# Performance work log

Measured on AMD Instinct MI355X. Metric: run time of the kernel, lower is better.

Reference implementation:

```python
import jax, jax.numpy as jnp
import numpy as np

B, S, D, H, I, E, K, L, C = 4, 1024, 512, 8, 2048, 8, 2, 4, 4
D2 = D // 2
EPS = 1e-5  # torch LayerNorm default


def _ln(x, w, b):
    m = jnp.mean(x, -1, keepdims=True)
    v = jnp.mean((x - m) ** 2, -1, keepdims=True)
    return (x - m) * jax.lax.rsqrt(v + EPS) * w + b


def setup_inputs() -> dict:
    key = jax.random.key(0)
    ks = iter(jax.random.split(key, 40))
    n = lambda shp, s=0.02: jax.random.normal(next(ks), shp, dtype=jnp.float32) * s
    return {
        'embeddings': jax.random.normal(next(ks), (B, S, D), jnp.float32),
        'attention_mask': jnp.ones((B, S), jnp.float32),
        'in_w': n((L, 3 * D, D)), 'in_b': jnp.zeros((L, 3 * D)),
        'out_w': n((L, D, D)), 'out_b': jnp.zeros((L, D)),
        'ln1_w': jnp.ones((L, D)), 'ln1_b': jnp.zeros((L, D)),
        'ln2_w': jnp.ones((L, D)), 'ln2_b': jnp.zeros((L, D)),
        'gate_w': n((L, E, D)),
        'e_w1': n((L, E, D, I)), 'e_b1': jnp.zeros((L, E, I)),
        'e_w2': n((L, E, I, D)), 'e_b2': jnp.zeros((L, E, D)),
        'mln_w': jnp.ones((L, D)), 'mln_b': jnp.zeros((L, D)),
        'fln_w': jnp.ones((D,)), 'fln_b': jnp.zeros((D,)),
        'pool_w': n((D, D)), 'pool_b': jnp.zeros((D,)),
        'cls_w': n((C, D)), 'cls_b': jnp.zeros((C,)),
        'cf_w1': n((D2, D)), 'cf_b1': jnp.zeros((D2,)),
        'cf_w2': n((1, D2)), 'cf_b2': jnp.zeros((1,)),
    }


def _forward(embeddings, attention_mask, in_w, in_b, out_w, out_b, ln1_w, ln1_b,
             ln2_w, ln2_b, gate_w, e_w1, e_b1, e_w2, e_b2, mln_w, mln_b,
             fln_w, fln_b, pool_w, pool_b, cls_w, cls_b, cf_w1, cf_b1, cf_w2, cf_b2):
    x = embeddings
    dh = D // H
    total_aux = jnp.float32(0.0)
    for l in range(L):
        # --- self-attention (eval mode, dropout off) ---
        h = _ln(x, ln1_w[l], ln1_b[l])
        qkv = h @ in_w[l].T + in_b[l]                       # (B,S,3D)
        q, k, v = jnp.split(qkv, 3, axis=-1)
        q = q.reshape(B, S, H, dh).transpose(0, 2, 1, 3)
        k = k.reshape(B, S, H, dh).transpose(0, 2, 1, 3)
        v = v.reshape(B, S, H, dh).transpose(0, 2, 1, 3)
        scores = jnp.einsum('bhqd,bhkd->bhqk', q, k) / (dh ** 0.5)
        attn = jax.nn.softmax(scores, axis=-1)
        ctx = jnp.einsum('bhqk,bhkd->bhqd', attn, v).transpose(0, 2, 1, 3).reshape(B, S, D)
        x = x + (ctx @ out_w[l].T + out_b[l])
        # --- MoE FFN (residual is the post-norm2 tensor, per source) ---
        h = _ln(x, ln2_w[l], ln2_b[l])
        flat = h.reshape(-1, D)                             # (T,D)
        probs = jax.nn.softmax(flat @ gate_w[l].T, axis=-1) # (T,E)
        vals, idx = jax.lax.top_k(probs, K)                 # (T,K)
        vals = vals / vals.sum(-1, keepdims=True)
        onehot = jax.nn.one_hot(idx, E, dtype=flat.dtype)   # (T,K,E)
        comb = jnp.einsum('tk,tke->te', vals, onehot)       # (T,E) per-expert weight, 0 if not selected
        mid = jax.nn.gelu(jnp.einsum('td,edf->tef', flat, e_w1[l]) + e_b1[l], approximate=False)
        eout = jnp.einsum('tef,efd->ted', mid, e_w2[l]) + e_b2[l]
        moe_out = jnp.einsum('ted,te->td', eout, comb).reshape(B, S, D)
        moe_out = moe_out * attention_mask[..., None]
        x = _ln(h + moe_out, mln_w[l], mln_b[l])
        usage = onehot.sum((0, 1)) / flat.shape[0]
        total_aux = total_aux + jnp.mean((usage - 1.0 / E) ** 2)
    # --- head ---
    x = _ln(x, fln_w, fln_b)
    me = attention_mask[..., None]
    pooled = (x * me).sum(1) / jnp.maximum(me.sum(1), 1e-9)
    pooled = jnp.tanh(pooled @ pool_w.T + pool_b)
    logits = pooled @ cls_w.T + cls_b
    conf = jax.nn.sigmoid(jax.nn.relu(pooled @ cf_w1.T + cf_b1) @ cf_w2.T + cf_b2)
    return logits, total_aux / L, conf


def reference(embeddings, attention_mask, in_w, in_b, out_w, out_b, ln1_w, ln1_b,
              ln2_w, ln2_b, gate_w, e_w1, e_b1, e_w2, e_b2, mln_w, mln_b,
              fln_w, fln_b, pool_w, pool_b, cls_w, cls_b, cf_w1, cf_b1, cf_w2, cf_b2):
    return _forward(embeddings, attention_mask, in_w, in_b, out_w, out_b, ln1_w, ln1_b,
                    ln2_w, ln2_b, gate_w, e_w1, e_b1, e_w2, e_b2, mln_w, mln_b,
                    fln_w, fln_b, pool_w, pool_b, cls_w, cls_b, cf_w1, cf_b1, cf_w2, cf_b2)
```

## Files before the change

kernel.cpp:

```cpp
#include <hip/hip_runtime.h>
#include <math.h>

#define B_ 4
#define S_ 1024
#define D_ 512
#define H_ 8
#define DH_ 64
#define I_ 2048
#define E_ 8
#define L_ 4
#define T_ 4096

using bf16x8 = __attribute__((ext_vector_type(8))) __bf16;
using f32x4  = __attribute__((ext_vector_type(4))) float;

typedef __attribute__((address_space(1))) const void gvoid;
typedef __attribute__((address_space(3))) void lvoid;
__device__ __forceinline__ void gl_lds16(const void* g, void* l){
  __builtin_amdgcn_global_load_lds((gvoid*)g, (lvoid*)l, 16, 0, 0);
}

__device__ __forceinline__ float wred_sum(float v){
#pragma unroll
  for(int m=32;m>0;m>>=1) v += __shfl_xor(v, m, 64);
  return v;
}
__device__ __forceinline__ unsigned short f2bf(float f){
  unsigned x = __float_as_uint(f);
  unsigned r = (x + 0x7FFFu + ((x>>16)&1u)) >> 16;
  return (unsigned short)r;
}
__device__ __forceinline__ float bf2f(unsigned short u){
  return __uint_as_float(((unsigned)u)<<16);
}
__device__ __forceinline__ unsigned pk2(float a, float b){
  return (unsigned)f2bf(a) | ((unsigned)f2bf(b)<<16);
}

template<int BM, int BN, bool MOE, bool GATHER, bool OUT_BF16, int ACT, bool ADD_IN>
__global__ __launch_bounds__(512)
void gemm_k(const unsigned short* __restrict__ A, const unsigned short* __restrict__ Bv,
            void* Cp, const float* __restrict__ bias, const float* addin,
            int M, int N, int K, int lda, int ldb, int ldc,
            int hdiv, long sAb, long sAh, long sBb, long sBh, long sCb, long sCh,
            float scale,
            const int* __restrict__ moff, const int* __restrict__ mcnt,
            const int* __restrict__ rowtok, const int* __restrict__ btab,
            long sBe, int biasStride, int nby)
{
  constexpr int BK = 64;
  constexpr int WM = BM/2, WN = BN/4, FM = WM/16, FNN = WN/16;
  constexpr int RPC = 64;
  constexpr int SHPC = 4096;
  constexpr int NA = BM/RPC, NB = BN/RPC;
  __shared__ unsigned short As[2*BM*BK];
  __shared__ unsigned short Bs[2*BN*BK];

  const int tid = threadIdx.x, wid = tid>>6, lane = tid&63;
  const int wy = wid>>2, wx = wid&3, ln16 = lane&15;

  const int nwg = gridDim.x, cpx = nwg >> 3;
  const int lin = blockIdx.x;
  const int wg  = (lin & 7)*cpx + (lin >> 3);
  const int bxi = wg / nby, byi = wg % nby;

  int m0 = bxi*BM;
  const int n0 = byi*BN;

  float* Cf = nullptr; unsigned short* Ch = nullptr;
  const float* biasp = bias;
  const unsigned short* Bp = Bv;
  int seg = 0, cnt = M;

  if constexpr (MOE){
    int tv = btab[bxi];
    if (tv < 0) return;
    int e = tv>>8;
    m0 = (tv&255)*BM;
    seg = moff[e]; cnt = mcnt[e];
    Bp = Bv + (long)e*sBe;
    if constexpr (OUT_BF16) Ch = (unsigned short*)Cp; else Cf = (float*)Cp;
    if (biasp) biasp += (long)e*biasStride;
  } else {
    int z = blockIdx.z, zb = z/hdiv, zh = z%hdiv;
    A  += (long)zb*sAb + (long)zh*sAh;
    Bp += (long)zb*sBb + (long)zh*sBh;
    long coff = (long)zb*sCb + (long)zh*sCh;
    if constexpr (OUT_BF16) Ch = (unsigned short*)Cp + coff; else Cf = ((float*)Cp) + coff;
    if constexpr (ADD_IN) addin += coff;
  }

  const int srow = tid >> 3;
  const int scol = ((tid & 7) ^ (srow & 7)) * 8;
  long ga[NA], gb[NB];
#pragma unroll
  for (int j=0; j<NA; j++){
    int r = m0 + j*RPC + srow;
    if constexpr (MOE){
      r = min(r, cnt-1);
      long gr = GATHER ? (long)rowtok[seg+r] : (long)(seg+r);
      ga[j] = gr*lda + scol;
    } else {
      ga[j] = (long)min(r, M-1)*lda + scol;
    }
  }
#pragma unroll
  for (int j=0; j<NB; j++){
    int bn = min(n0 + j*RPC + srow, N-1);
    gb[j] = (long)bn*ldb + scol;
  }

  f32x4 acc[FM][FNN];
#pragma unroll
  for(int i=0;i<FM;i++)
#pragma unroll
    for(int j=0;j<FNN;j++){ f32x4 z = {0.f,0.f,0.f,0.f}; acc[i][j] = z; }

  const int nt = K/BK;
  const int rsw = ln16 & 7;
  const int u0 = ((lane>>4)     ^ rsw) * 8;
  const int u1 = ((4+(lane>>4)) ^ rsw) * 8;

#pragma unroll
  for (int j=0; j<NA; j++) gl_lds16(A + ga[j], As + j*SHPC + wid*512);
#pragma unroll
  for (int j=0; j<NB; j++) gl_lds16(Bp + gb[j], Bs + j*SHPC + wid*512);

  for (int t = 0; t < nt; ++t){
    const int cb = t & 1;
    const unsigned short* Ab = As + cb*BM*BK;
    const unsigned short* Bb = Bs + cb*BN*BK;
    unsigned short* An = As + (cb^1)*BM*BK;
    unsigned short* Bn = Bs + (cb^1)*BN*BK;
    const bool pf = (t+1 < nt);
    const long k0n = (long)(t+1)*BK;

    asm volatile("s_waitcnt vmcnt(0)" ::: "memory");
    __builtin_amdgcn_s_barrier();
    __builtin_amdgcn_sched_barrier(0);

    if (pf){
#pragma unroll
      for (int j=0; j<NA; j++) gl_lds16(A + ga[j] + k0n, An + j*SHPC + wid*512);
    }
    {
      bf16x8 fa[FM], fb[FNN];
#pragma unroll
      for(int i=0;i<FM;i++) fa[i] = *(const bf16x8*)&Ab[(wy*WM + i*16 + ln16)*BK + u0];
#pragma unroll
      for(int j=0;j<FNN;j++) fb[j] = *(const bf16x8*)&Bb[(wx*WN + j*16 + ln16)*BK + u0];
      __builtin_amdgcn_s_setprio(1);
#pragma unroll
      for(int i=0;i<FM;i++)
#pragma unroll
        for(int j=0;j<FNN;j++)
          acc[i][j] = __builtin_amdgcn_mfma_f32_16x16x32_bf16(fa[i], fb[j], acc[i][j], 0, 0, 0);
      __builtin_amdgcn_s_setprio(0);
    }
    if (pf){
#pragma unroll
      for (int j=0; j<NB; j++) gl_lds16(Bp + gb[j] + k0n, Bn + j*SHPC + wid*512);
    }
    {
      bf16x8 fa[FM], fb[FNN];
#pragma unroll
      for(int i=0;i<FM;i++) fa[i] = *(const bf16x8*)&Ab[(wy*WM + i*16 + ln16)*BK + u1];
#pragma unroll
      for(int j=0;j<FNN;j++) fb[j] = *(const bf16x8*)&Bb[(wx*WN + j*16 + ln16)*BK + u1];
      __builtin_amdgcn_s_setprio(1);
#pragma unroll
      for(int i=0;i<FM;i++)
#pragma unroll
        for(int j=0;j<FNN;j++)
          acc[i][j] = __builtin_amdgcn_mfma_f32_16x16x32_bf16(fa[i], fb[j], acc[i][j], 0, 0, 0);
      __builtin_amdgcn_s_setprio(0);
    }
  }

#pragma unroll
  for(int i=0;i<FM;i++){
    int mbase = m0 + wy*WM + i*16 + (lane>>4)*4;
#pragma unroll
    for(int j=0;j<FNN;j++){
      int n = n0 + wx*WN + j*16 + ln16;
      float bv = biasp ? biasp[n] : 0.f;
      f32x4 v = acc[i][j];
#pragma unroll
      for(int r=0;r<4;r++){
        int m = mbase + r;
        if (m < cnt){
          float x = v[r]*scale + bv;
          if constexpr (ACT == 1) x = 0.5f*x*(1.f + erff(x*0.70710678118654752f));
          long ci = (long)(MOE ? seg + m : m)*ldc + n;
          if constexpr (ADD_IN) x += addin[ci];
          if constexpr (OUT_BF16) Ch[ci] = f2bf(x);
          else Cf[ci] = x;
        }
      }
    }
  }
}

__global__ __launch_bounds__(256)
void flash_k(const unsigned short* __restrict__ qkvb, const unsigned short* __restrict__ Vt,
             unsigned short* __restrict__ ctx)
{
  __shared__ unsigned short Pl[4][16*72];
  const int qt = blockIdx.x, z = blockIdx.y, b = z>>3, h = z&7;
  const int wid = threadIdx.x>>6, lane = threadIdx.x&63;
  const int ln16 = lane&15, g = lane>>4;
  const int q0 = qt*64 + wid*16;
  unsigned short* Pw = &Pl[wid][0];

  const unsigned short* Qp = qkvb + (long)(b*1024 + q0 + ln16)*1536 + h*64 + g*8;
  bf16x8 qf0 = *(const bf16x8*)Qp;
  bf16x8 qf1 = *(const bf16x8*)(Qp + 32);
  const unsigned short* Kbase = qkvb + (long)b*1024*1536 + 512 + h*64 + g*8;
  const unsigned short* Vbase = Vt + (long)z*65536 + g*8;

  float m_s[4], l_s[4];
  f32x4 oacc[4];
#pragma unroll
  for(int r=0;r<4;r++){ m_s[r] = -1e30f; l_s[r] = 0.f; }
#pragma unroll
  for(int j=0;j<4;j++){ f32x4 zz = {0.f,0.f,0.f,0.f}; oacc[j] = zz; }

  for (int t = 0; t < 16; ++t){
    bf16x8 kf[4][2], vf[4][2];
#pragma unroll
    for(int j=0;j<4;j++){
      const unsigned short* kp = Kbase + (long)(t*64 + j*16 + ln16)*1536;
      kf[j][0] = *(const bf16x8*)kp;
      kf[j][1] = *(const bf16x8*)(kp + 32);
      const unsigned short* vp = Vbase + (long)(j*16 + ln16)*1024 + t*64;
      vf[j][0] = *(const bf16x8*)vp;
      vf[j][1] = *(const bf16x8*)(vp + 32);
    }
    f32x4 sacc[4];
#pragma unroll
    for(int j=0;j<4;j++){ f32x4 zz = {0.f,0.f,0.f,0.f}; sacc[j] = zz; }
#pragma unroll
    for(int j=0;j<4;j++){
      sacc[j] = __builtin_amdgcn_mfma_f32_16x16x32_bf16(qf0, kf[j][0], sacc[j], 0,0,0);
      sacc[j] = __builtin_amdgcn_mfma_f32_16x16x32_bf16(qf1, kf[j][1], sacc[j], 0,0,0);
    }
#pragma unroll
    for(int j=0;j<4;j++)
#pragma unroll
      for(int r=0;r<4;r++) sacc[j][r] *= 0.125f;
    float alpha[4];
#pragma unroll
    for(int r=0;r<4;r++){
      float mx = fmaxf(fmaxf(sacc[0][r], sacc[1][r]), fmaxf(sacc[2][r], sacc[3][r]));
#pragma unroll
      for(int m=1;m<16;m<<=1) mx = fmaxf(mx, __shfl_xor(mx, m, 64));
      float mn = fmaxf(m_s[r], mx);
      alpha[r] = __expf(m_s[r] - mn);
      m_s[r] = mn;
    }
#pragma unroll
    for(int j=0;j<4;j++)
#pragma unroll
      for(int r=0;r<4;r++) sacc[j][r] = __expf(sacc[j][r] - m_s[r]);
#pragma unroll
    for(int r=0;r<4;r++){
      float rs = sacc[0][r]+sacc[1][r]+sacc[2][r]+sacc[3][r];
#pragma unroll
      for(int m=1;m<16;m<<=1) rs += __shfl_xor(rs, m, 64);
      l_s[r] = l_s[r]*alpha[r] + rs;
    }
#pragma unroll
    for(int j=0;j<4;j++)
#pragma unroll
      for(int r=0;r<4;r++) oacc[j][r] *= alpha[r];
#pragma unroll
    for(int j=0;j<4;j++)
#pragma unroll
      for(int r=0;r<4;r++)
        Pw[(g*4+r)*72 + j*16 + ln16] = f2bf(sacc[j][r]);
    bf16x8 pf0 = *(const bf16x8*)&Pw[ln16*72 + g*8];
    bf16x8 pf1 = *(const bf16x8*)&Pw[ln16*72 + 32 + g*8];
#pragma unroll
    for(int j=0;j<4;j++){
      oacc[j] = __builtin_amdgcn_mfma_f32_16x16x32_bf16(pf0, vf[j][0], oacc[j], 0,0,0);
      oacc[j] = __builtin_amdgcn_mfma_f32_16x16x32_bf16(pf1, vf[j][1], oacc[j], 0,0,0);
    }
  }
#pragma unroll
  for(int r=0;r<4;r++){
    float inv = 1.f/l_s[r];
    long row = (long)(b*1024 + q0 + g*4 + r)*512 + h*64;
#pragma unroll
    for(int j=0;j<4;j++)
      ctx[row + j*16 + ln16] = f2bf(oacc[j][r]*inv);
  }
}

template<bool OUT_BF16>
__global__ __launch_bounds__(256)
void ln_w_k(const float* __restrict__ in, const float* __restrict__ w,
            const float* __restrict__ bb, void* __restrict__ outp)
{
  int row = blockIdx.x*4 + (threadIdx.x>>6), lane = threadIdx.x&63;
  const float4* p = (const float4*)(in + (long)row*512 + lane*8);
  float4 a = p[0], c = p[1];
  float s = a.x+a.y+a.z+a.w + c.x+c.y+c.z+c.w;
  float q = a.x*a.x+a.y*a.y+a.z*a.z+a.w*a.w + c.x*c.x+c.y*c.y+c.z*c.z+c.w*c.w;
  s = wred_sum(s); q = wred_sum(q);
  float mean = s*(1.f/512.f);
  float var  = q*(1.f/512.f) - mean*mean;
  float inv  = rsqrtf(var + 1e-5f);
  const float4* wp = (const float4*)(w + lane*8);
  const float4* bp = (const float4*)(bb + lane*8);
  float4 w0 = wp[0], w1 = wp[1], b0 = bp[0], b1 = bp[1];
  float o0 = (a.x-mean)*inv*w0.x + b0.x, o1 = (a.y-mean)*inv*w0.y + b0.y;
  float o2 = (a.z-mean)*inv*w0.z + b0.z, o3 = (a.w-mean)*inv*w0.w + b0.w;
  float o4 = (c.x-mean)*inv*w1.x + b1.x, o5 = (c.y-mean)*inv*w1.y + b1.y;
  float o6 = (c.z-mean)*inv*w1.z + b1.z, o7 = (c.w-mean)*inv*w1.w + b1.w;
  if constexpr (OUT_BF16){
    *(uint4*)((unsigned short*)outp + (long)row*512 + lane*8) =
      make_uint4(pk2(o0,o1), pk2(o2,o3), pk2(o4,o5), pk2(o6,o7));
  } else {
    float4* op = (float4*)((float*)outp + (long)row*512 + lane*8);
    op[0] = make_float4(o0,o1,o2,o3);
    op[1] = make_float4(o4,o5,o6,o7);
  }
}

__global__ __launch_bounds__(256)
void ln2route_k(const float* __restrict__ in, const float* __restrict__ w,
                const float* __restrict__ bb, unsigned short* __restrict__ h2,
                const float* __restrict__ gw,
                int* __restrict__ tok_e, float* __restrict__ tok_w)
{
  int tok = blockIdx.x*4 + (threadIdx.x>>6), lane = threadIdx.x&63;
  const float4* p = (const float4*)(in + (long)tok*512 + lane*8);
  float4 a = p[0], c = p[1];
  float s = a.x+a.y+a.z+a.w + c.x+c.y+c.z+c.w;
  float q = a.x*a.x+a.y*a.y+a.z*a.z+a.w*a.w + c.x*c.x+c.y*c.y+c.z*c.z+c.w*c.w;
  s = wred_sum(s); q = wred_sum(q);
  float mean = s*(1.f/512.f);
  float var  = q*(1.f/512.f) - mean*mean;
  float inv  = rsqrtf(var + 1e-5f);
  const float4* wp = (const float4*)(w + lane*8);
  const float4* bp = (const float4*)(bb + lane*8);
  float4 w0 = wp[0], w1 = wp[1], b0 = bp[0], b1 = bp[1];
  float o[8];
  o[0] = (a.x-mean)*inv*w0.x + b0.x; o[1] = (a.y-mean)*inv*w0.y + b0.y;
  o[2] = (a.z-mean)*inv*w0.z + b0.z; o[3] = (a.w-mean)*inv*w0.w + b0.w;
  o[4] = (c.x-mean)*inv*w1.x + b1.x; o[5] = (c.y-mean)*inv*w1.y + b1.y;
  o[6] = (c.z-mean)*inv*w1.z + b1.z; o[7] = (c.w-mean)*inv*w1.w + b1.w;
  *(uint4*)(h2 + (long)tok*512 + lane*8) =
    make_uint4(pk2(o[0],o[1]), pk2(o[2],o[3]), pk2(o[4],o[5]), pk2(o[6],o[7]));
  float lg[8];
#pragma unroll
  for(int e=0;e<8;e++){
    const float4* gr = (const float4*)(gw + e*512 + lane*8);
    float4 g0 = gr[0], g1 = gr[1];
    float d = o[0]*g0.x + o[1]*g0.y + o[2]*g0.z + o[3]*g0.w
            + o[4]*g1.x + o[5]*g1.y + o[6]*g1.z + o[7]*g1.w;
    lg[e] = wred_sum(d);
  }
  if (lane == 0){
    float mx = lg[0];
#pragma unroll
    for(int e=1;e<8;e++) mx = fmaxf(mx, lg[e]);
    float pr[8];
#pragma unroll
    for(int e=0;e<8;e++) pr[e] = expf(lg[e]-mx);
    int e0 = 0; float p0 = pr[0];
#pragma unroll
    for(int e=1;e<8;e++) if (pr[e] > p0){ p0 = pr[e]; e0 = e; }
    int e1 = -1; float p1 = -1.f;
#pragma unroll
    for(int e=0;e<8;e++) if (e != e0 && pr[e] > p1){ p1 = pr[e]; e1 = e; }
    float invp = 1.f/(p0+p1);
    tok_e[2*tok] = e0; tok_e[2*tok+1] = e1;
    tok_w[2*tok] = p0*invp; tok_w[2*tok+1] = p1*invp;
  }
}

__global__ __launch_bounds__(1024)
void plan_scatter_k(const int* __restrict__ tok_e, const float* __restrict__ tok_w,
                    int* __restrict__ offs, int* __restrict__ cnts, float* __restrict__ aux,
                    int* __restrict__ btab, int* __restrict__ btab64,
                    int* __restrict__ rowtok, float* __restrict__ roww, int* __restrict__ rowof)
{
  __shared__ int hist[8];
  __shared__ int offsS[8];
  __shared__ int base[8];
  const int t = threadIdx.x;
  if (t < 8) hist[t] = 0;
  __syncthreads();
  int e[8]; float w[8];
#pragma unroll
  for (int i=0;i<8;i++){
    e[i] = tok_e[t + i*1024];
    w[i] = tok_w[t + i*1024];
    atomicAdd(&hist[e[i]], 1);
  }
  __syncthreads();
  if (t == 0){
    int o = 0, idx = 0, idx2 = 0; float a = 0.f;
    for (int ee=0; ee<8; ee++){
      offsS[ee] = o;
      int c = hist[ee];
      o += c;
      float u = (float)c*(1.f/4096.f) - 0.125f;
      a += u*u;
      int nb = (c + 127) >> 7;
      for (int j=0;j<nb;j++) btab[idx++] = (ee<<8)|j;
      int nb2 = (c + 63) >> 6;
      for (int j=0;j<nb2;j++) btab64[idx2++] = (ee<<8)|j;
    }
    while (idx < 80) btab[idx++] = -1;
    while (idx2 < 144) btab64[idx2++] = -1;
    *aux += a*(1.f/8.f);
  }
  __syncthreads();
  if (t < 8){
    cnts[t] = hist[t];
    offs[t] = offsS[t];
    base[t] = offsS[t];
  }
  __syncthreads();
#pragma unroll
  for (int i=0;i<8;i++){
    int pos = atomicAdd(&base[e[i]], 1);
    int gi = t + i*1024;
    rowtok[pos] = gi>>1;
    roww[pos] = w[i];
    rowof[gi] = pos;
  }
}

__global__ __launch_bounds__(256)
void ln_moe_k(const float* __restrict__ eout, const int* __restrict__ rowof,
              const float* __restrict__ roww, const float* __restrict__ mask,
              const unsigned short* __restrict__ h2,
              const float* __restrict__ w, const float* __restrict__ bb,
              float* __restrict__ outp)
{
  int tok = blockIdx.x*4 + (threadIdx.x>>6), lane = threadIdx.x&63;
  int r0 = rowof[2*tok], r1 = rowof[2*tok+1];
  float w0w = roww[r0], w1w = roww[r1], mk = mask[tok];
  const float4* ap = (const float4*)(eout + (long)r0*512 + lane*8);
  const float4* bp2 = (const float4*)(eout + (long)r1*512 + lane*8);
  float4 a0 = ap[0], a1 = ap[1], c0 = bp2[0], c1 = bp2[1];
  uint4 hu = *(const uint4*)(h2 + (long)tok*512 + lane*8);
  const unsigned short* hh = (const unsigned short*)&hu;
  float v[8];
  v[0] = bf2f(hh[0]) + (a0.x*w0w + c0.x*w1w)*mk;
  v[1] = bf2f(hh[1]) + (a0.y*w0w + c0.y*w1w)*mk;
  v[2] = bf2f(hh[2]) + (a0.z*w0w + c0.z*w1w)*mk;
  v[3] = bf2f(hh[3]) + (a0.w*w0w + c0.w*w1w)*mk;
  v[4] = bf2f(hh[4]) + (a1.x*w0w + c1.x*w1w)*mk;
  v[5] = bf2f(hh[5]) + (a1.y*w0w + c1.y*w1w)*mk;
  v[6] = bf2f(hh[6]) + (a1.z*w0w + c1.z*w1w)*mk;
  v[7] = bf2f(hh[7]) + (a1.w*w0w + c1.w*w1w)*mk;
  float s = 0.f, q = 0.f;
#pragma unroll
  for(int i=0;i<8;i++){ s += v[i]; q += v[i]*v[i]; }
  s = wred_sum(s); q = wred_sum(q);
  float mean = s*(1.f/512.f);
  float var  = q*(1.f/512.f) - mean*mean;
  float inv  = rsqrtf(var + 1e-5f);
  const float4* wp = (const float4*)(w + lane*8);
  const float4* bpp = (const float4*)(bb + lane*8);
  float4 w0 = wp[0], w1 = wp[1], b0 = bpp[0], b1 = bpp[1];
  float wv[8] = {w0.x,w0.y,w0.z,w0.w,w1.x,w1.y,w1.z,w1.w};
  float bv[8] = {b0.x,b0.y,b0.z,b0.w,b1.x,b1.y,b1.z,b1.w};
  float4* op = (float4*)(outp + (long)tok*512 + lane*8);
  op[0] = make_float4((v[0]-mean)*inv*wv[0]+bv[0], (v[1]-mean)*inv*wv[1]+bv[1],
                      (v[2]-mean)*inv*wv[2]+bv[2], (v[3]-mean)*inv*wv[3]+bv[3]);
  op[1] = make_float4((v[4]-mean)*inv*wv[4]+bv[4], (v[5]-mean)*inv*wv[5]+bv[5],
                      (v[6]-mean)*inv*wv[6]+bv[6], (v[7]-mean)*inv*wv[7]+bv[7]);
}

__global__ __launch_bounds__(256)
void vt_k(const unsigned short* __restrict__ qkvb, unsigned short* __restrict__ Vt)
{
  __shared__ unsigned short tile[64][80];
  int z = blockIdx.y, b = z>>3, h = z&7;
  int t = threadIdx.x;
  int kk = t>>2, dd = (t&3)*16;
  int dd2 = t>>2, kk2 = (t&3)*16;
  for (int c = 0; c < 4; ++c){
    int k0 = (blockIdx.x*4 + c)*64;
    const unsigned short* p = qkvb + ((long)(b*1024 + k0 + kk))*1536 + 1024 + h*64 + dd;
    uint4 u0 = *(const uint4*)p, u1 = *(const uint4*)(p+8);
    __syncthreads();
    *(uint4*)&tile[kk][dd] = u0;
    *(uint4*)&tile[kk][dd+8] = u1;
    __syncthreads();
    uint4 o0, o1;
    unsigned short* s0 = (unsigned short*)&o0;
    unsigned short* s1 = (unsigned short*)&o1;
#pragma unroll
    for(int j=0;j<8;j++){ s0[j] = tile[kk2+j][dd2]; s1[j] = tile[kk2+8+j][dd2]; }
    unsigned short* o = Vt + (long)z*65536 + (long)dd2*1024 + k0 + kk2;
    *(uint4*)o = o0; *(uint4*)(o+8) = o1;
  }
}

__global__ __launch_bounds__(256)
void transpose_cast_k(const float* __restrict__ in, unsigned short* __restrict__ outp,
                      int R, int C, int ZL)
{
  __shared__ float tile[64][65];
  int t = threadIdx.x;
  int rr = t>>2, cc = (t&3)*16;
  int cc2 = t>>2, rr2 = (t&3)*16;
  int c0 = blockIdx.x*64, r0 = blockIdx.y*64;
  for (int zi = 0; zi < ZL; ++zi){
    long zoff = (long)(blockIdx.z*ZL + zi) * R * C;
    const float* pin = in + zoff + (long)(r0+rr)*C + c0 + cc;
    float4 v0=*(const float4*)pin, v1=*(const float4*)(pin+4), v2=*(const float4*)(pin+8), v3=*(const float4*)(pin+12);
    __syncthreads();
    tile[rr][cc+0]=v0.x; tile[rr][cc+1]=v0.y; tile[rr][cc+2]=v0.z; tile[rr][cc+3]=v0.w;
    tile[rr][cc+4]=v1.x; tile[rr][cc+5]=v1.y; tile[rr][cc+6]=v1.z; tile[rr][cc+7]=v1.w;
    tile[rr][cc+8]=v2.x; tile[rr][cc+9]=v2.y; tile[rr][cc+10]=v2.z; tile[rr][cc+11]=v2.w;
    tile[rr][cc+12]=v3.x; tile[rr][cc+13]=v3.y; tile[rr][cc+14]=v3.z; tile[rr][cc+15]=v3.w;
    __syncthreads();
    unsigned tmp[8];
#pragma unroll
    for(int jj=0;jj<8;jj++)
      tmp[jj] = pk2(tile[rr2+2*jj][cc2], tile[rr2+2*jj+1][cc2]);
    uint4* dst = (uint4*)(outp + zoff + (long)(c0+cc2)*R + r0 + rr2);
    dst[0] = make_uint4(tmp[0],tmp[1],tmp[2],tmp[3]);
    dst[1] = make_uint4(tmp[4],tmp[5],tmp[6],tmp[7]);
  }
}

__global__ __launch_bounds__(256)
void cast_bf16_k(const float* __restrict__ in, unsigned short* __restrict__ outp, int n8)
{
  for (int i = blockIdx.x*256 + threadIdx.x; i < n8; i += gridDim.x*256){
    const float4* p = (const float4*)(in + (long)i*8);
    float4 a = p[0], b = p[1];
    *(uint4*)(outp + (long)i*8) = make_uint4(pk2(a.x,a.y), pk2(a.z,a.w), pk2(b.x,b.y), pk2(b.z,b.w));
  }
}

__global__ __launch_bounds__(256)
void pool2_k(const float* __restrict__ h, const float* __restrict__ mask, float* __restrict__ pooled)
{
  int b = blockIdx.x, sc = blockIdx.y, t = threadIdx.x;
  float a0 = 0.f, a1 = 0.f;
  const float* mb = mask + b*1024 + sc*128;
  const float* hbase = h + ((long)b*1024 + sc*128)*512;
  for (int s = 0; s < 128; ++s){
    float mk = mb[s];
    const float* r = hbase + (long)s*512;
    a0 += r[t]*mk; a1 += r[t+256]*mk;
  }
  pooled[((b*8 + sc)*512) + t] = a0;
  pooled[((b*8 + sc)*512) + t + 256] = a1;
}

__global__ __launch_bounds__(256)
void head_final_k(const float* __restrict__ pooled, const float* __restrict__ mask,
                  const float* __restrict__ pool_w, const float* __restrict__ pool_b,
                  const float* __restrict__ cls_w, const float* __restrict__ cls_b,
                  const float* __restrict__ cf_w1, const float* __restrict__ cf_b1,
                  const float* __restrict__ cf_w2, const float* __restrict__ cf_b2,
                  const float* __restrict__ aux, float* __restrict__ out)
{
  int b = blockIdx.x, t = threadIdx.x, wid = t>>6, lane = t&63;
  __shared__ __align__(16) float pld[512];
  __shared__ __align__(16) float p2[512];
  __shared__ float red[4];
  float ds = 0.f;
  for(int s=t; s<1024; s+=256) ds += mask[b*1024 + s];
  ds = wred_sum(ds);
  if (lane==0) red[wid] = ds;
  __syncthreads();
  float denom = fmaxf(red[0]+red[1]+red[2]+red[3], 1e-9f);
  float s0 = 0.f, s1 = 0.f;
#pragma unroll
  for(int sc=0;sc<8;sc++){
    s0 += pooled[((b*8+sc)*512) + t];
    s1 += pooled[((b*8+sc)*512) + t + 256];
  }
  pld[t]     = s0/denom;
  pld[t+256] = s1/denom;
  __syncthreads();
#pragma unroll
  for(int jj=0;jj<2;jj++){
    int j = t + jj*256;
    const float4* wr = (const float4*)(pool_w + (long)j*512);
    float acc = 0.f;
    for(int i=0;i<128;i++){
      float4 w4 = wr[i]; float4 x4 = ((const float4*)pld)[i];
      acc += w4.x*x4.x + w4.y*x4.y + w4.z*x4.z + w4.w*x4.w;
    }
    p2[j] = tanhf(acc + pool_b[j]);
  }
  __syncthreads();
  if (t < 4){
    const float4* wr = (const float4*)(cls_w + (long)t*512);
    float acc = 0.f;
    for(int i=0;i<128;i++){
      float4 w4 = wr[i]; float4 x4 = ((const float4*)p2)[i];
      acc += w4.x*x4.x + w4.y*x4.y + w4.z*x4.z + w4.w*x4.w;
    }
    out[b*4 + t] = acc + cls_b[t];
  }
  {
    const float4* wr = (const float4*)(cf_w1 + (long)t*512);
    float acc = 0.f;
    for(int i=0;i<128;i++){
      float4 w4 = wr[i]; float4 x4 = ((const float4*)p2)[i];
      acc += w4.x*x4.x + w4.y*x4.y + w4.z*x4.z + w4.w*x4.w;
    }
    acc = fmaxf(acc + cf_b1[t], 0.f) * cf_w2[t];
    acc = wred_sum(acc);
    __syncthreads();
    if (lane==0) red[wid] = acc;
    __syncthreads();
    if (t == 0){
      float sum = red[0]+red[1]+red[2]+red[3];
      out[17 + b] = 1.f/(1.f + expf(-(sum + cf_b2[0])));
    }
  }
  if (b == 0 && t == 0) out[16] = aux[0]*0.25f;
}

extern "C" void kernel_launch(void* const* d_in, const int* in_sizes, int n_in,
                              void* d_out, int out_size, void* d_ws, size_t ws_size,
                              hipStream_t stream)
{
  (void)in_sizes; (void)n_in; (void)out_size;
  const float* emb    = (const float*)d_in[0];
  const float* mask   = (const float*)d_in[1];
  const float* in_w   = (const float*)d_in[2];
  const float* in_b   = (const float*)d_in[3];
  const float* out_w  = (const float*)d_in[4];
  const float* out_b  = (const float*)d_in[5];
  const float* ln1_w  = (const float*)d_in[6];
  const float* ln1_b  = (const float*)d_in[7];
  const float* ln2_w  = (const float*)d_in[8];
  const float* ln2_b  = (const float*)d_in[9];
  const float* gate_w = (const float*)d_in[10];
  const float* e_w1   = (const float*)d_in[11];
  const float* e_b1   = (const float*)d_in[12];
  const float* e_w2   = (const float*)d_in[13];
  const float* e_b2   = (const float*)d_in[14];
  const float* mln_w  = (const float*)d_in[15];
  const float* mln_b  = (const float*)d_in[16];
  const float* fln_w  = (const float*)d_in[17];
  const float* fln_b  = (const float*)d_in[18];
  const float* pool_w = (const float*)d_in[19];
  const float* pool_b = (const float*)d_in[20];
  const float* cls_w  = (const float*)d_in[21];
  const float* cls_b  = (const float*)d_in[22];
  const float* cf_w1  = (const float*)d_in[23];
  const float* cf_b1  = (const float*)d_in[24];
  const float* cf_w2  = (const float*)d_in[25];
  const float* cf_b2  = (const float*)d_in[26];
  float* out = (float*)d_out;
  char* ws = (char*)d_ws;

  const size_t MiB = 1024*1024;
  if (ws_size < 218*MiB) return;

  float*          x     = (float*)(ws + 0*MiB);
  unsigned short* hb    = (unsigned short*)(ws + 8*MiB);
  unsigned short* qkvb  = (unsigned short*)(ws + 12*MiB);
  unsigned short* ctx   = (unsigned short*)(ws + 24*MiB);
  unsigned short* Vt    = (unsigned short*)(ws + 28*MiB);
  unsigned short* mid   = (unsigned short*)(ws + 32*MiB);
  float*          eout  = (float*)(ws + 64*MiB);
  float*          fout  = (float*)(ws + 64*MiB);
  unsigned short* w1t   = (unsigned short*)(ws + 80*MiB);
  unsigned short* w2t   = (unsigned short*)(ws + 144*MiB);
  unsigned short* inwb  = (unsigned short*)(ws + 208*MiB);
  unsigned short* outwb = (unsigned short*)(ws + 214*MiB);
  char* misc = ws + 216*MiB;
  int*   counts  = (int*)(misc + 0);
  int*   offs    = (int*)(misc + 64);
  float* aux     = (float*)(misc + 128);
  int*   btab    = (int*)(misc + 256);
  int*   btab64  = (int*)(misc + 1024);
  float* pooled  = (float*)(misc + 4096);
  int*   tok_e   = (int*)(misc + 81920);
  float* tok_w   = (float*)(misc + 114688);
  int*   rowtok  = (int*)(misc + 147456);
  float* roww    = (float*)(misc + 180224);
  int*   rowof   = (int*)(misc + 212992);

  hipMemcpyAsync(x, emb, (size_t)T_*D_*4, hipMemcpyDeviceToDevice, stream);
  hipMemsetAsync(aux, 0, 4, stream);
  cast_bf16_k<<<512, 256, 0, stream>>>(in_w, inwb, L_*3*D_*D_/8);
  cast_bf16_k<<<256, 256, 0, stream>>>(out_w, outwb, L_*D_*D_/8);
  transpose_cast_k<<<dim3(I_/64, D_/64, 4), 256, 0, stream>>>(e_w1, w1t, D_, I_, 8);
  transpose_cast_k<<<dim3(D_/64, I_/64, 4), 256, 0, stream>>>(e_w2, w2t, I_, D_, 8);

  for (int l=0; l<L_; l++){
    const float* inbl  = in_b  + (size_t)l*3*D_;
    const float* outbl = out_b + (size_t)l*D_;
    const float* gwl   = gate_w + (size_t)l*E_*D_;
    const float* eb1l  = e_b1 + (size_t)l*E_*I_;
    const float* eb2l  = e_b2 + (size_t)l*E_*D_;
    const unsigned short* inwbl  = inwb + (size_t)l*3*D_*D_;
    const unsigned short* outwbl = outwb + (size_t)l*D_*D_;
    const unsigned short* w1tl = w1t + (size_t)l*E_*I_*D_;
    const unsigned short* w2tl = w2t + (size_t)l*E_*D_*I_;

    ln_w_k<true><<<T_/4, 256, 0, stream>>>(x, ln1_w + (size_t)l*D_, ln1_b + (size_t)l*D_, hb);
    gemm_k<64,128,false,false,true,0,false><<<dim3(768,1,1), 512, 0, stream>>>(
      hb, inwbl, qkvb, inbl, nullptr, T_, 3*D_, D_, D_, D_, 3*D_,
      1, 0,0,0,0,0,0, 1.f, nullptr, nullptr, nullptr, nullptr, 0, 0, 12);
    vt_k<<<dim3(4,32), 256, 0, stream>>>(qkvb, Vt);
    flash_k<<<dim3(16,32), 256, 0, stream>>>(qkvb, Vt, ctx);
    gemm_k<64,64,false,false,false,0,true><<<dim3(512,1,1), 512, 0, stream>>>(
      ctx, outwbl, x, outbl, x, T_, D_, D_, D_, D_, D_,
      1, 0,0,0,0,0,0, 1.f, nullptr, nullptr, nullptr, nullptr, 0, 0, 8);
    ln2route_k<<<T_/4, 256, 0, stream>>>(x, ln2_w + (size_t)l*D_, ln2_b + (size_t)l*D_,
                                         hb, gwl, tok_e, tok_w);
    plan_scatter_k<<<1, 1024, 0, stream>>>(tok_e, tok_w, offs, counts, aux, btab, btab64,
                                           rowtok, roww, rowof);
    gemm_k<128,128,true,true,true,1,false><<<dim3(1136,1,1), 512, 0, stream>>>(
      hb, w1tl, mid, eb1l, nullptr, 2*T_, I_, D_, D_, D_, I_,
      1, 0,0,0,0,0,0, 1.f, offs, counts, rowtok, btab, (long)I_*D_, I_, 16);
    gemm_k<64,128,true,false,false,0,false><<<dim3(544,1,1), 512, 0, stream>>>(
      mid, w2tl, eout, eb2l, nullptr, 2*T_, D_, I_, I_, I_, D_,
      1, 0,0,0,0,0,0, 1.f, offs, counts, nullptr, btab64, (long)D_*I_, D_, 4);
    ln_moe_k<<<T_/4, 256, 0, stream>>>(eout, rowof, roww, mask, hb,
                                       mln_w + (size_t)l*D_, mln_b + (size_t)l*D_, x);
  }
  ln_w_k<false><<<T_/4, 256, 0, stream>>>(x, fln_w, fln_b, fout);
  pool2_k<<<dim3(4,8), 256, 0, stream>>>(fout, mask, pooled);
  head_final_k<<<4, 256, 0, stream>>>(pooled, mask, pool_w, pool_b, cls_w, cls_b,
                                      cf_w1, cf_b1, cf_w2, cf_b2, aux, out);
}
```

Before: 1.326 ms.

## Fuse next-layer LayerNorm into MoE epilogue and retile expert up-projection GEMM

The post-MoE LayerNorm kernel now also applies the next layer's pre-attention LayerNorm, or the final LayerNorm on the last layer. It writes that result straight into the bf16 activation buffer, or the final fp32 output, which removes a separate LN launch and its reread of x each layer. The first layer's LN1 is hoisted before the loop and reads the embeddings directly. Separately, the expert up-projection GEMM switches from 128x128 to 128x64 tiles with a doubled grid, trading per-tile reuse for more parallelism. The fused kernel reads and writes hb in the same thread, which relies on each thread reading its row before overwriting it.

```diff
diff --git a/kernel.cpp b/kernel.cpp
--- a/kernel.cpp
+++ b/kernel.cpp
@@ -434,12 +434,15 @@
   }
 }
 
+template<bool OUT2_BF16>
 __global__ __launch_bounds__(256)
 void ln_moe_k(const float* __restrict__ eout, const int* __restrict__ rowof,
               const float* __restrict__ roww, const float* __restrict__ mask,
               const unsigned short* __restrict__ h2,
               const float* __restrict__ w, const float* __restrict__ bb,
-              float* __restrict__ outp)
+              float* __restrict__ outp,
+              const float* __restrict__ w2, const float* __restrict__ b2,
+              void* __restrict__ out2)
 {
   int tok = blockIdx.x*4 + (threadIdx.x>>6), lane = threadIdx.x&63;
   int r0 = rowof[2*tok], r1 = rowof[2*tok+1];
@@ -470,11 +473,35 @@
   float4 w0 = wp[0], w1 = wp[1], b0 = bpp[0], b1 = bpp[1];
   float wv[8] = {w0.x,w0.y,w0.z,w0.w,w1.x,w1.y,w1.z,w1.w};
   float bv[8] = {b0.x,b0.y,b0.z,b0.w,b1.x,b1.y,b1.z,b1.w};
+  float o[8];
+#pragma unroll
+  for(int i=0;i<8;i++) o[i] = (v[i]-mean)*inv*wv[i]+bv[i];
   float4* op = (float4*)(outp + (long)tok*512 + lane*8);
-  op[0] = make_float4((v[0]-mean)*inv*wv[0]+bv[0], (v[1]-mean)*inv*wv[1]+bv[1],
-                      (v[2]-mean)*inv*wv[2]+bv[2], (v[3]-mean)*inv*wv[3]+bv[3]);
-  op[1] = make_float4((v[4]-mean)*inv*wv[4]+bv[4], (v[5]-mean)*inv*wv[5]+bv[5],
-                      (v[6]-mean)*inv*wv[6]+bv[6], (v[7]-mean)*inv*wv[7]+bv[7]);
+  op[0] = make_float4(o[0], o[1], o[2], o[3]);
+  op[1] = make_float4(o[4], o[5], o[6], o[7]);
+  float s2 = 0.f, q2 = 0.f;
+#pragma unroll
+  for(int i=0;i<8;i++){ s2 += o[i]; q2 += o[i]*o[i]; }
+  s2 = wred_sum(s2); q2 = wred_sum(q2);
+  float mean2 = s2*(1.f/512.f);
+  float var2  = q2*(1.f/512.f) - mean2*mean2;
+  float inv2  = rsqrtf(var2 + 1e-5f);
+  const float4* wp2 = (const float4*)(w2 + lane*8);
+  const float4* bp3 = (const float4*)(b2 + lane*8);
+  float4 x0 = wp2[0], x1 = wp2[1], y0 = bp3[0], y1 = bp3[1];
+  float wv2[8] = {x0.x,x0.y,x0.z,x0.w,x1.x,x1.y,x1.z,x1.w};
+  float bv2[8] = {y0.x,y0.y,y0.z,y0.w,y1.x,y1.y,y1.z,y1.w};
+  float o2[8];
+#pragma unroll
+  for(int i=0;i<8;i++) o2[i] = (o[i]-mean2)*inv2*wv2[i]+bv2[i];
+  if constexpr (OUT2_BF16){
+    *(uint4*)((unsigned short*)out2 + (long)tok*512 + lane*8) =
+      make_uint4(pk2(o2[0],o2[1]), pk2(o2[2],o2[3]), pk2(o2[4],o2[5]), pk2(o2[6],o2[7]));
+  } else {
+    float4* op2 = (float4*)((float*)out2 + (long)tok*512 + lane*8);
+    op2[0] = make_float4(o2[0], o2[1], o2[2], o2[3]);
+    op2[1] = make_float4(o2[4], o2[5], o2[6], o2[7]);
+  }
 }
 
 __global__ __launch_bounds__(256)
@@ -696,6 +723,8 @@
   transpose_cast_k<<<dim3(I_/64, D_/64, 4), 256, 0, stream>>>(e_w1, w1t, D_, I_, 8);
   transpose_cast_k<<<dim3(D_/64, I_/64, 4), 256, 0, stream>>>(e_w2, w2t, I_, D_, 8);
 
+  ln_w_k<true><<<T_/4, 256, 0, stream>>>(emb, ln1_w, ln1_b, hb);
+
   for (int l=0; l<L_; l++){
     const float* inbl  = in_b  + (size_t)l*3*D_;
     const float* outbl = out_b + (size_t)l*D_;
@@ -707,7 +736,6 @@
     const unsigned short* w1tl = w1t + (size_t)l*E_*I_*D_;
     const unsigned short* w2tl = w2t + (size_t)l*E_*D_*I_;
 
-    ln_w_k<true><<<T_/4, 256, 0, stream>>>(x, ln1_w + (size_t)l*D_, ln1_b + (size_t)l*D_, hb);
     gemm_k<64,128,false,false,true,0,false><<<dim3(768,1,1), 512, 0, stream>>>(
       hb, inwbl, qkvb, inbl, nullptr, T_, 3*D_, D_, D_, D_, 3*D_,
       1, 0,0,0,0,0,0, 1.f, nullptr, nullptr, nullptr, nullptr, 0, 0, 12);
@@ -720,16 +748,23 @@
                                          hb, gwl, tok_e, tok_w);
     plan_scatter_k<<<1, 1024, 0, stream>>>(tok_e, tok_w, offs, counts, aux, btab, btab64,
                                            rowtok, roww, rowof);
-    gemm_k<128,128,true,true,true,1,false><<<dim3(1136,1,1), 512, 0, stream>>>(
+    gemm_k<128,64,true,true,true,1,false><<<dim3(2272,1,1), 512, 0, stream>>>(
       hb, w1tl, mid, eb1l, nullptr, 2*T_, I_, D_, D_, D_, I_,
-      1, 0,0,0,0,0,0, 1.f, offs, counts, rowtok, btab, (long)I_*D_, I_, 16);
+      1, 0,0,0,0,0,0, 1.f, offs, counts, rowtok, btab, (long)I_*D_, I_, 32);
     gemm_k<64,128,true,false,false,0,false><<<dim3(544,1,1), 512, 0, stream>>>(
       mid, w2tl, eout, eb2l, nullptr, 2*T_, D_, I_, I_, I_, D_,
       1, 0,0,0,0,0,0, 1.f, offs, counts, nullptr, btab64, (long)D_*I_, D_, 4);
-    ln_moe_k<<<T_/4, 256, 0, stream>>>(eout, rowof, roww, mask, hb,
-                                       mln_w + (size_t)l*D_, mln_b + (size_t)l*D_, x);
-  }
-  ln_w_k<false><<<T_/4, 256, 0, stream>>>(x, fln_w, fln_b, fout);
+    if (l < 3){
+      ln_moe_k<true><<<T_/4, 256, 0, stream>>>(eout, rowof, roww, mask, hb,
+                                               mln_w + (size_t)l*D_, mln_b + (size_t)l*D_, x,
+                                               ln1_w + (size_t)(l+1)*D_, ln1_b + (size_t)(l+1)*D_,
+                                               (void*)hb);
+    } else {
+      ln_moe_k<false><<<T_/4, 256, 0, stream>>>(eout, rowof, roww, mask, hb,
+                                                mln_w + (size_t)l*D_, mln_b + (size_t)l*D_, x,
+                                                fln_w, fln_b, (void*)fout);
+    }
+  }
   pool2_k<<<dim3(4,8), 256, 0, stream>>>(fout, mask, pooled);
   head_final_k<<<4, 256, 0, stream>>>(pooled, mask, pool_w, pool_b, cls_w, cls_b,
                                       cf_w1, cf_b1, cf_w2, cf_b2, aux, out);
```

Result: faster. 1.294 ms (-2.5%).
